# Kernel optimization log

Hardware: AMD Instinct MI355X
Metric: run time of the kernel (lower is better)

## Reference

```python
import jax, jax.numpy as jnp
import numpy as np


def setup_inputs() -> dict:
    key = jax.random.key(0)
    ks = jax.random.split(key, 5)
    B, T, C, HS = 8, 2048, 1024, 64
    return {
        "x_q": jax.random.normal(ks[0], (B, T, C), dtype=jnp.float32),
        "x_kv": jax.random.normal(ks[1], (B, T, C), dtype=jnp.float32),
        "Wq": jax.random.normal(ks[2], (C, HS), dtype=jnp.float32) * (C ** -0.5),
        "Wk": jax.random.normal(ks[3], (C, HS), dtype=jnp.float32) * (C ** -0.5),
        "Wv": jax.random.normal(ks[4], (C, HS), dtype=jnp.float32) * (C ** -0.5),
    }


def reference(x_q, x_kv, Wq, Wk, Wv):
    # x_q, x_kv: [B, T, C]; W*: [C, HS]
    B, T, C = x_q.shape
    q = jnp.einsum("btc,ch->bth", x_q, Wq)   # [B, T, HS]
    k = jnp.einsum("btc,ch->bth", x_kv, Wk)  # [B, T, HS]
    v = jnp.einsum("btc,ch->bth", x_kv, Wv)  # [B, T, HS]
    # NOTE: original scales by d_model**-0.5 (C), not head_size**-0.5
    wei = jnp.einsum("bqh,bkh->bqk", q, k) * (C ** -0.5)  # [B, T, T]
    causal = jnp.tril(jnp.ones((T, T), dtype=bool))
    wei = jnp.where(causal, wei, -jnp.inf)
    wei = jax.nn.softmax(wei, axis=-1)
    out = jnp.einsum("bqk,bkh->bqh", wei, v)  # [B, T, HS]
    return out
```

## Files before the change

### kernel.cpp

```cpp
#include <hip/hip_runtime.h>

typedef __bf16 bf16_t;
typedef __bf16 bf16x8 __attribute__((ext_vector_type(8)));
typedef float f32x4 __attribute__((ext_vector_type(4)));
typedef unsigned short u16x4 __attribute__((ext_vector_type(4)));

#define B_ 8
#define T_ 2048
#define C_ 1024
#define HS_ 64
#define VSTRIDE 2080

#define MFMA __builtin_amdgcn_mfma_f32_16x16x32_bf16

__device__ __forceinline__ float fast_exp2(float x) {
#if __has_builtin(__builtin_amdgcn_exp2f)
  return __builtin_amdgcn_exp2f(x);
#else
  return exp2f(x);
#endif
}

__device__ __forceinline__ void async_ld16(const float* gsrc, float* lds_dst) {
  __builtin_amdgcn_global_load_lds(
      (const __attribute__((address_space(1))) void*)gsrc,
      (__attribute__((address_space(3))) void*)lds_dst, 16, 0, 0);
}

__global__ __launch_bounds__(256) void repack_w(
    const float* __restrict__ Wq, const float* __restrict__ Wk,
    const float* __restrict__ Wv, bf16_t* __restrict__ pq,
    bf16_t* __restrict__ pk, bf16_t* __restrict__ pv) {
  const float* W = (blockIdx.y == 0) ? Wq : ((blockIdx.y == 1) ? Wk : Wv);
  bf16_t* P = (blockIdx.y == 0) ? pq : ((blockIdx.y == 1) ? pk : pv);
  int t = blockIdx.x * 256 + threadIdx.x;
  int lane = t & 63, nt = (t >> 6) & 3, kc = t >> 8;
  int quad = lane >> 4, ln = lane & 15;
  bf16x8 v;
#pragma unroll
  for (int j = 0; j < 8; ++j)
    v[j] = (bf16_t)W[(kc * 32 + quad * 8 + j) * HS_ + nt * 16 + ln];
  *(bf16x8*)(P + (size_t)t * 8) = v;
}

__global__ __launch_bounds__(256) void proj_mfma(
    const float* __restrict__ xq, const float* __restrict__ xkv,
    const bf16_t* __restrict__ pq, const bf16_t* __restrict__ pk,
    const bf16_t* __restrict__ pv, bf16_t* __restrict__ q,
    bf16_t* __restrict__ k, bf16_t* __restrict__ vT) {
  __shared__ float Xb[64][260];

  const int rt = blockIdx.x;
  const bool is_kv = (blockIdx.y != 0);
  const int w = threadIdx.x >> 6, lane = threadIdx.x & 63;
  const int quad = lane >> 4, ln = lane & 15;
  const int m0blk = rt * 64;
  const int m0 = m0blk + w * 16;
  const float* x = is_kv ? xkv : xq;
  const bf16_t* p0 = is_kv ? pk : pq;

  f32x4 acc0[4], acc1[4];
#pragma unroll
  for (int nt = 0; nt < 4; ++nt) {
    acc0[nt] = (f32x4){0.f, 0.f, 0.f, 0.f};
    acc1[nt] = (f32x4){0.f, 0.f, 0.f, 0.f};
  }

  for (int c = 0; c < 4; ++c) {
#pragma unroll
    for (int i = 0; i < 16; ++i) {
      const int row = w * 16 + i;
      async_ld16(x + (size_t)(m0blk + row) * C_ + c * 256 + lane * 4,
                 &Xb[row][0]);
    }
    asm volatile("s_waitcnt vmcnt(0)" ::: "memory");

#pragma unroll 2
    for (int kc2 = 0; kc2 < 8; ++kc2) {
      const int kcg = c * 8 + kc2;
      f32x4 xlo = *(const f32x4*)&Xb[w * 16 + ln][kc2 * 32 + quad * 8];
      f32x4 xhi = *(const f32x4*)&Xb[w * 16 + ln][kc2 * 32 + quad * 8 + 4];
      bf16x8 a;
#pragma unroll
      for (int j = 0; j < 4; ++j) {
        a[j] = (bf16_t)xlo[j];
        a[4 + j] = (bf16_t)xhi[j];
      }
#pragma unroll
      for (int nt = 0; nt < 4; ++nt) {
        bf16x8 b = *(const bf16x8*)(p0 + ((size_t)(kcg * 4 + nt) * 64 + lane) * 8);
        acc0[nt] = MFMA(a, b, acc0[nt], 0, 0, 0);
      }
      if (is_kv) {
#pragma unroll
        for (int nt = 0; nt < 4; ++nt) {
          bf16x8 b = *(const bf16x8*)(pv + ((size_t)(kcg * 4 + nt) * 64 + lane) * 8);
          acc1[nt] = MFMA(a, b, acc1[nt], 0, 0, 0);
        }
      }
    }
    asm volatile("" ::: "memory");
  }

  if (!is_kv) {
#pragma unroll
    for (int nt = 0; nt < 4; ++nt)
#pragma unroll
      for (int r = 0; r < 4; ++r)
        q[(size_t)(m0 + quad * 4 + r) * HS_ + nt * 16 + ln] = (bf16_t)acc0[nt][r];
  } else {
#pragma unroll
    for (int nt = 0; nt < 4; ++nt)
#pragma unroll
      for (int r = 0; r < 4; ++r)
        k[(size_t)(m0 + quad * 4 + r) * HS_ + nt * 16 + ln] = (bf16_t)acc0[nt][r];
    const int bb = m0 >> 11, t0 = m0 & (T_ - 1);
#pragma unroll
    for (int nt = 0; nt < 4; ++nt) {
      u16x4 pk4;
#pragma unroll
      for (int r = 0; r < 4; ++r) {
        bf16_t h = (bf16_t)acc1[nt][r];
        pk4[r] = *(unsigned short*)&h;
      }
      *(u16x4*)((unsigned short*)vT + ((size_t)(bb * HS_ + nt * 16 + ln)) * VSTRIDE +
                t0 + quad * 4) = pk4;
    }
  }
}

__global__ __launch_bounds__(512) void attn_mfma(
    const bf16_t* __restrict__ q, const bf16_t* __restrict__ k,
    const bf16_t* __restrict__ vT, float* __restrict__ out) {
  __shared__ bf16_t p_lds[8][16][80];
  __shared__ float o_buf[8][16][66];
  __shared__ float l_buf[8][16][17];

  const int b = blockIdx.x >> 7;
  const int gq = blockIdx.x & 127;
  const int w = threadIdx.x >> 6, lane = threadIdx.x & 63;
  const int quad = lane >> 4, ln = lane & 15;
  const int qr0 = gq * 16;
  const size_t bt = (size_t)b * T_;
  const int td = gq >> 2;

  bf16x8 aq[2];
#pragma unroll
  for (int hc = 0; hc < 2; ++hc)
    aq[hc] = *(const bf16x8*)(q + (bt + qr0 + ln) * HS_ + hc * 32 + quad * 8);

  f32x4 o_acc[4];
  float l_part[4] = {0.f, 0.f, 0.f, 0.f};
#pragma unroll
  for (int nt = 0; nt < 4; ++nt) o_acc[nt] = (f32x4){0.f, 0.f, 0.f, 0.f};
  const float scl = 0.03125f * 1.44269504088896340736f;

  for (int t = w; t <= td; t += 8) {
    const int kr0 = t * 64;

    f32x4 s[4];
#pragma unroll
    for (int nt = 0; nt < 4; ++nt) s[nt] = (f32x4){0.f, 0.f, 0.f, 0.f};
#pragma unroll
    for (int hc = 0; hc < 2; ++hc)
#pragma unroll
      for (int nt = 0; nt < 4; ++nt) {
        bf16x8 bk = *(const bf16x8*)(k + (bt + kr0 + nt * 16 + ln) * HS_ +
                                     hc * 32 + quad * 8);
        s[nt] = MFMA(aq[hc], bk, s[nt], 0, 0, 0);
      }

    const bool diag = (t == td);
#pragma unroll
    for (int nt = 0; nt < 4; ++nt)
#pragma unroll
      for (int r = 0; r < 4; ++r) {
        float e = fast_exp2(s[nt][r] * scl);
        if (diag && (kr0 + nt * 16 + ln > qr0 + quad * 4 + r)) e = 0.f;
        l_part[r] += e;
        p_lds[w][quad * 4 + r][nt * 16 + ln] = (bf16_t)e;
      }

#pragma unroll
    for (int kc = 0; kc < 2; ++kc) {
      bf16x8 ap = *(const bf16x8*)&p_lds[w][ln][kc * 32 + quad * 8];
#pragma unroll
      for (int nt = 0; nt < 4; ++nt) {
        bf16x8 bv = *(const bf16x8*)(vT +
                                     ((size_t)(b * HS_ + nt * 16 + ln)) * VSTRIDE +
                                     kr0 + kc * 32 + quad * 8);
        o_acc[nt] = MFMA(ap, bv, o_acc[nt], 0, 0, 0);
      }
    }
  }

#pragma unroll
  for (int nt = 0; nt < 4; ++nt)
#pragma unroll
    for (int r = 0; r < 4; ++r)
      o_buf[w][quad * 4 + r][nt * 16 + ln] = o_acc[nt][r];
#pragma unroll
  for (int r = 0; r < 4; ++r) l_buf[w][quad * 4 + r][ln] = l_part[r];
  __syncthreads();

#pragma unroll
  for (int rr = 0; rr < 2; ++rr) {
    const int row = w + rr * 8;
    float o = 0.f, lsum = 0.f;
#pragma unroll
    for (int ww = 0; ww < 8; ++ww) {
      o += o_buf[ww][row][lane];
      lsum += l_buf[ww][row][lane & 15];
    }
#pragma unroll
    for (int off = 1; off < 16; off <<= 1) lsum += __shfl_xor(lsum, off);
    out[(bt + qr0 + row) * HS_ + lane] = o / lsum;
  }
}

extern "C" void kernel_launch(void* const* d_in, const int* in_sizes, int n_in,
                              void* d_out, int out_size, void* d_ws,
                              size_t ws_size, hipStream_t stream) {
  (void)in_sizes; (void)n_in; (void)out_size; (void)ws_size;
  const float* xq = (const float*)d_in[0];
  const float* xkv = (const float*)d_in[1];
  const float* Wq = (const float*)d_in[2];
  const float* Wk = (const float*)d_in[3];
  const float* Wv = (const float*)d_in[4];
  float* out = (float*)d_out;

  char* ws = (char*)d_ws;
  bf16_t* q = (bf16_t*)ws;
  bf16_t* kk = (bf16_t*)(ws + (2u << 20));
  bf16_t* vT = (bf16_t*)(ws + (4u << 20));
  bf16_t* pq = (bf16_t*)(ws + (6656u << 10));
  bf16_t* pk = (bf16_t*)(ws + (6784u << 10));
  bf16_t* pv = (bf16_t*)(ws + (6912u << 10));

  repack_w<<<dim3(32, 3), 256, 0, stream>>>(Wq, Wk, Wv, pq, pk, pv);
  proj_mfma<<<dim3(256, 2), 256, 0, stream>>>(xq, xkv, pq, pk, pv, q, kk, vT);
  attn_mfma<<<dim3(1024), 512, 0, stream>>>(q, kk, vT, out);
}
```

Measured before the change: 218.7 us.

## Double-buffer projection loads with swizzled LDS and staged weight tiles

The projection kernel is restructured into a double-buffered pipeline. It stages 128-column chunks of X together with the packed weight tiles into LDS via async global-to-LDS loads, using partial vmcnt waits so the next chunk loads while the current one computes. An XOR swizzle on the X rows is meant to reduce LDS bank conflicts. The q and kv variants become separate template instantiations in two launches, which removes the runtime branch but serializes the two grids and adds barrier overhead.

```diff
diff --git a/kernel.cpp b/kernel.cpp
--- a/kernel.cpp
+++ b/kernel.cpp
@@ -21,7 +21,7 @@
 #endif
 }
 
-__device__ __forceinline__ void async_ld16(const float* gsrc, float* lds_dst) {
+__device__ __forceinline__ void async_ld16(const void* gsrc, void* lds_dst) {
   __builtin_amdgcn_global_load_lds(
       (const __attribute__((address_space(1))) void*)gsrc,
       (__attribute__((address_space(3))) void*)lds_dst, 16, 0, 0);
@@ -43,21 +43,19 @@
   *(bf16x8*)(P + (size_t)t * 8) = v;
 }
 
+template <bool KV>
 __global__ __launch_bounds__(256) void proj_mfma(
-    const float* __restrict__ xq, const float* __restrict__ xkv,
-    const bf16_t* __restrict__ pq, const bf16_t* __restrict__ pk,
-    const bf16_t* __restrict__ pv, bf16_t* __restrict__ q,
-    bf16_t* __restrict__ k, bf16_t* __restrict__ vT) {
-  __shared__ float Xb[64][260];
-
-  const int rt = blockIdx.x;
-  const bool is_kv = (blockIdx.y != 0);
+    const float* __restrict__ x, const bf16_t* __restrict__ pA,
+    const bf16_t* __restrict__ pB, bf16_t* __restrict__ outA,
+    bf16_t* __restrict__ vT) {
+  __shared__ float Xb[2][64][128];
+  __shared__ bf16_t Bb[2][KV ? 2 : 1][16][512];
+
   const int w = threadIdx.x >> 6, lane = threadIdx.x & 63;
   const int quad = lane >> 4, ln = lane & 15;
-  const int m0blk = rt * 64;
+  const int m0blk = blockIdx.x * 64;
   const int m0 = m0blk + w * 16;
-  const float* x = is_kv ? xkv : xq;
-  const bf16_t* p0 = is_kv ? pk : pq;
+  const int l32 = lane & 31, lhalf = lane >> 5;
 
   f32x4 acc0[4], acc1[4];
 #pragma unroll
@@ -66,20 +64,37 @@
     acc1[nt] = (f32x4){0.f, 0.f, 0.f, 0.f};
   }
 
-  for (int c = 0; c < 4; ++c) {
-#pragma unroll
-    for (int i = 0; i < 16; ++i) {
-      const int row = w * 16 + i;
-      async_ld16(x + (size_t)(m0blk + row) * C_ + c * 256 + lane * 4,
-                 &Xb[row][0]);
-    }
-    asm volatile("s_waitcnt vmcnt(0)" ::: "memory");
-
-#pragma unroll 2
-    for (int kc2 = 0; kc2 < 8; ++kc2) {
-      const int kcg = c * 8 + kc2;
-      f32x4 xlo = *(const f32x4*)&Xb[w * 16 + ln][kc2 * 32 + quad * 8];
-      f32x4 xhi = *(const f32x4*)&Xb[w * 16 + ln][kc2 * 32 + quad * 8 + 4];
+  auto STAGE = [&](int c, int buf) {
+#pragma unroll
+    for (int i = 0; i < 8; ++i) {
+      const int row = w * 16 + 2 * i + lhalf;
+      const int sg = l32 ^ (row & 7);
+      async_ld16(x + (size_t)(m0blk + row) * C_ + c * 128 + sg * 4,
+                 &Xb[buf][w * 16 + 2 * i][0]);
+    }
+#pragma unroll
+    for (int j = 0; j < 4; ++j) {
+      const int p = w * 4 + j;
+      async_ld16(pA + (size_t)(c * 16 + p) * 512 + lane * 8,
+                 &Bb[buf][0][p][0]);
+    }
+    if constexpr (KV) {
+#pragma unroll
+      for (int j = 0; j < 4; ++j) {
+        const int p = w * 4 + j;
+        async_ld16(pB + (size_t)(c * 16 + p) * 512 + lane * 8,
+                   &Bb[buf][1][p][0]);
+      }
+    }
+  };
+
+  auto COMPUTE = [&](int c, int buf) {
+    const int swz = (ln & 7) << 4;
+    const char* rp = (const char*)&Xb[buf][w * 16 + ln][0];
+#pragma unroll
+    for (int kc2 = 0; kc2 < 4; ++kc2) {
+      f32x4 xlo = *(const f32x4*)(rp + ((kc2 * 128 + quad * 32) ^ swz));
+      f32x4 xhi = *(const f32x4*)(rp + ((kc2 * 128 + quad * 32 + 16) ^ swz));
       bf16x8 a;
 #pragma unroll
       for (int j = 0; j < 4; ++j) {
@@ -88,32 +103,65 @@
       }
 #pragma unroll
       for (int nt = 0; nt < 4; ++nt) {
-        bf16x8 b = *(const bf16x8*)(p0 + ((size_t)(kcg * 4 + nt) * 64 + lane) * 8);
-        acc0[nt] = MFMA(a, b, acc0[nt], 0, 0, 0);
-      }
-      if (is_kv) {
+        bf16x8 b0 = *(const bf16x8*)&Bb[buf][0][kc2 * 4 + nt][lane * 8];
+        acc0[nt] = MFMA(a, b0, acc0[nt], 0, 0, 0);
+      }
+      if constexpr (KV) {
 #pragma unroll
         for (int nt = 0; nt < 4; ++nt) {
-          bf16x8 b = *(const bf16x8*)(pv + ((size_t)(kcg * 4 + nt) * 64 + lane) * 8);
-          acc1[nt] = MFMA(a, b, acc1[nt], 0, 0, 0);
+          bf16x8 b1 = *(const bf16x8*)&Bb[buf][1][kc2 * 4 + nt][lane * 8];
+          acc1[nt] = MFMA(a, b1, acc1[nt], 0, 0, 0);
         }
       }
     }
-    asm volatile("" ::: "memory");
-  }
-
-  if (!is_kv) {
+  };
+
+#define WAIT_CHUNK()                                        \
+  do {                                                      \
+    if constexpr (KV)                                       \
+      asm volatile("s_waitcnt vmcnt(16)" ::: "memory");     \
+    else                                                    \
+      asm volatile("s_waitcnt vmcnt(12)" ::: "memory");     \
+  } while (0)
+
+  STAGE(0, 0);
+  STAGE(1, 1);
+  WAIT_CHUNK();
+  __builtin_amdgcn_s_barrier();
+  __builtin_amdgcn_sched_barrier(0);
+
+#pragma unroll
+  for (int c = 0; c < 8; ++c) {
+    COMPUTE(c, c & 1);
+    if (c == 7) break;
+    asm volatile("s_waitcnt lgkmcnt(0)" ::: "memory");
+    __builtin_amdgcn_s_barrier();
+    __builtin_amdgcn_sched_barrier(0);
+    if (c < 6) {
+      STAGE(c + 2, c & 1);
+      WAIT_CHUNK();
+    } else {
+      asm volatile("s_waitcnt vmcnt(0)" ::: "memory");
+    }
+    __builtin_amdgcn_s_barrier();
+    __builtin_amdgcn_sched_barrier(0);
+  }
+#undef WAIT_CHUNK
+
+  if constexpr (!KV) {
 #pragma unroll
     for (int nt = 0; nt < 4; ++nt)
 #pragma unroll
       for (int r = 0; r < 4; ++r)
-        q[(size_t)(m0 + quad * 4 + r) * HS_ + nt * 16 + ln] = (bf16_t)acc0[nt][r];
+        outA[(size_t)(m0 + quad * 4 + r) * HS_ + nt * 16 + ln] =
+            (bf16_t)acc0[nt][r];
   } else {
 #pragma unroll
     for (int nt = 0; nt < 4; ++nt)
 #pragma unroll
       for (int r = 0; r < 4; ++r)
-        k[(size_t)(m0 + quad * 4 + r) * HS_ + nt * 16 + ln] = (bf16_t)acc0[nt][r];
+        outA[(size_t)(m0 + quad * 4 + r) * HS_ + nt * 16 + ln] =
+            (bf16_t)acc0[nt][r];
     const int bb = m0 >> 11, t0 = m0 & (T_ - 1);
 #pragma unroll
     for (int nt = 0; nt < 4; ++nt) {
@@ -123,8 +171,9 @@
         bf16_t h = (bf16_t)acc1[nt][r];
         pk4[r] = *(unsigned short*)&h;
       }
-      *(u16x4*)((unsigned short*)vT + ((size_t)(bb * HS_ + nt * 16 + ln)) * VSTRIDE +
-                t0 + quad * 4) = pk4;
+      *(u16x4*)((unsigned short*)vT +
+                ((size_t)(bb * HS_ + nt * 16 + ln)) * VSTRIDE + t0 + quad * 4) =
+          pk4;
     }
   }
 }
@@ -238,6 +287,7 @@
   bf16_t* pv = (bf16_t*)(ws + (6912u << 10));
 
   repack_w<<<dim3(32, 3), 256, 0, stream>>>(Wq, Wk, Wv, pq, pk, pv);
-  proj_mfma<<<dim3(256, 2), 256, 0, stream>>>(xq, xkv, pq, pk, pv, q, kk, vT);
+  proj_mfma<false><<<dim3(256), 256, 0, stream>>>(xq, pq, nullptr, q, nullptr);
+  proj_mfma<true><<<dim3(256), 256, 0, stream>>>(xkv, pk, pv, kk, vT);
   attn_mfma<<<dim3(1024), 512, 0, stream>>>(q, kk, vT, out);
 }
```

Measured after the change: 206.6 us. 5.5% less time.
